# Optimization experiments

Hardware: AMD Instinct MI355X
Metric: run time of the kernel (lower is better)

## Reference

```python
import jax, jax.numpy as jnp
import numpy as np

N_NODES = 50000
N_EDGES = 800000
D_IN = 64
D_HID = 256
BN_EPS = 1e-5


def setup_inputs() -> dict:
    key = jax.random.key(0)
    ks = jax.random.split(key, 8)
    s = 1.0 / np.sqrt(D_IN)
    sg = 1.0 / np.sqrt(D_HID)
    return {
        "xs": jax.random.normal(ks[0], (N_NODES, D_IN), jnp.float32),
        "edge_index": jax.random.randint(ks[1], (2, N_EDGES), 0, N_NODES, jnp.int64),
        "W_gcn": jax.random.normal(ks[2], (D_IN, D_HID), jnp.float32) * s,
        "b_gcn": jnp.zeros((D_HID,), jnp.float32),
        "W_lin": jax.random.normal(ks[3], (D_IN, D_HID), jnp.float32) * s,
        "b_lin": jnp.zeros((D_HID,), jnp.float32),
        "W_gate": jax.random.normal(ks[4], (D_HID, D_HID), jnp.float32) * sg,
        "b_gate": jnp.zeros((D_HID,), jnp.float32),
        "bn_gamma": jnp.ones((D_HID,), jnp.float32),
        "bn_beta": jnp.zeros((D_HID,), jnp.float32),
    }


def reference(xs, edge_index, W_gcn, b_gcn, W_lin, b_lin, W_gate, b_gate, bn_gamma, bn_beta):
    N = xs.shape[0]
    # --- GCNConv: add self loops, symmetric normalization D^-1/2 (A+I) D^-1/2 ---
    loops = jnp.arange(N, dtype=edge_index.dtype)
    src = jnp.concatenate([edge_index[0], loops])  # message sources
    dst = jnp.concatenate([edge_index[1], loops])  # aggregation targets
    deg = jax.ops.segment_sum(jnp.ones(src.shape, jnp.float32), dst, num_segments=N)
    dinv = jax.lax.rsqrt(jnp.maximum(deg, 1.0))  # deg >= 1 due to self loops
    norm = dinv[src] * dinv[dst]                 # [E+N]
    h = xs @ W_gcn                               # [N, D_HID]
    z = jax.ops.segment_sum(h[src] * norm[:, None], dst, num_segments=N) + b_gcn
    z = jnp.tanh(z)
    # --- gating + linear residual ---
    g = jax.nn.sigmoid(z @ W_gate + b_gate)
    xl = xs @ W_lin + b_lin
    out = jax.nn.relu((1.0 - g) * xl + g * z)
    # --- BatchNorm over nodes (training-mode batch statistics) ---
    mu = out.mean(axis=0)
    var = out.var(axis=0)
    out = (out - mu) * jax.lax.rsqrt(var + BN_EPS) * bn_gamma + bn_beta
    # dropout is identity in eval mode
    return out
```

## Files before the change

kernel.cpp:

```cpp
#include <hip/hip_runtime.h>
#include <math.h>

#define NN 50000
#define NE 800000
#define D_IN 64
#define D_HID 256
#define BN_EPS 1e-5f
#define ZSTR 264
#define SB 128
#define BCAP 64

typedef __attribute__((ext_vector_type(8))) short short8;
typedef __attribute__((ext_vector_type(4))) float f32x4;

static __device__ __forceinline__ unsigned short f2bf(float f) {
    unsigned int u = __builtin_bit_cast(unsigned int, f);
    u += 0x7FFFu + ((u >> 16) & 1u);
    return (unsigned short)(u >> 16);
}
static __device__ __forceinline__ float bf2f(unsigned short s) {
    unsigned int u = ((unsigned int)s) << 16;
    return __builtin_bit_cast(float, u);
}
static __device__ __forceinline__ float fast_sigmoid(float x) {
    return __builtin_amdgcn_rcpf(1.0f + __expf(-x));
}
static __device__ __forceinline__ float fast_tanh(float x) {
    return 1.0f - 2.0f * __builtin_amdgcn_rcpf(__expf(2.0f * x) + 1.0f);
}

static __device__ __forceinline__ long a_addr(int i, int k) {
    return ((long)((i >> 4) * 2 + (k >> 5)) << 9) + ((((k >> 3) & 3) * 16 + (i & 15)) << 3) + (k & 7);
}

__global__ __launch_bounds__(256) void k_pre(const float* __restrict__ W_gcn,
                      const float* __restrict__ W_lin, const float* __restrict__ W_gate,
                      unsigned short* __restrict__ Wp_gcn, unsigned short* __restrict__ Wp_lin,
                      unsigned short* __restrict__ Wp_gate,
                      const int* __restrict__ eidx, int* __restrict__ cnt,
                      unsigned short* __restrict__ csr, int E) {
    int idx = blockIdx.x * blockDim.x + threadIdx.x;
    if (idx < 98304) {
        const float* W;
        unsigned short* Wp;
        int KC, o;
        if (idx < 16384)      { W = W_gcn;  Wp = Wp_gcn;  KC = 2; o = idx; }
        else if (idx < 32768) { W = W_lin;  Wp = Wp_lin;  KC = 2; o = idx - 16384; }
        else                  { W = W_gate; Wp = Wp_gate; KC = 8; o = idx - 32768; }
        int j = o & 7;
        int lane = (o >> 3) & 63;
        int rest = o >> 9;
        int kc = rest % KC;
        int ct = rest / KC;
        int col = ct * 16 + (lane & 15);
        int k = kc * 32 + (lane >> 4) * 8 + j;
        Wp[o] = f2bf(W[k * D_HID + col]);
    }
    if (idx * 4 < E) {
        int4 s = *(const int4*)(eidx + idx * 4);
        int4 d = *(const int4*)(eidx + E + idx * 4);
        int r0 = atomicAdd(&cnt[d.x], 1);
        int r1 = atomicAdd(&cnt[d.y], 1);
        int r2 = atomicAdd(&cnt[d.z], 1);
        int r3 = atomicAdd(&cnt[d.w], 1);
        if (r0 < BCAP) csr[d.x * BCAP + r0] = (unsigned short)s.x;
        if (r1 < BCAP) csr[d.y * BCAP + r1] = (unsigned short)s.y;
        if (r2 < BCAP) csr[d.z * BCAP + r2] = (unsigned short)s.z;
        if (r3 < BCAP) csr[d.w * BCAP + r3] = (unsigned short)s.w;
    }
}

__global__ __launch_bounds__(256) void k_prep(const float* __restrict__ xs,
                           const int* __restrict__ cnt,
                           float* __restrict__ dinv, unsigned short* __restrict__ xscaled,
                           unsigned short* __restrict__ xs_p, int n) {
    int idx = blockIdx.x * blockDim.x + threadIdx.x;
    if (idx >= n * 8) {
        if (idx < n * 8 + 8) {
            short8 zv = (short8){0, 0, 0, 0, 0, 0, 0, 0};
            *(short8*)(xscaled + (long)n * D_IN + (idx - n * 8) * 8) = zv;
        }
        return;
    }
    int i = idx >> 3;
    int sub = idx & 7;
    float dv = rsqrtf(1.0f + (float)cnt[i]);
    if (sub == 0) dinv[i] = dv;
    const float* p = xs + (long)i * D_IN + sub * 8;
    float4 f0 = *(const float4*)p;
    float4 f1 = *(const float4*)(p + 4);
    float vals[8] = {f0.x, f0.y, f0.z, f0.w, f1.x, f1.y, f1.z, f1.w};
    short8 xsc, xsb;
#pragma unroll
    for (int j = 0; j < 8; j++) {
        xsc[j] = (short)f2bf(vals[j] * dv);
        xsb[j] = (short)f2bf(vals[j]);
    }
    *(short8*)(xscaled + (long)i * D_IN + sub * 8) = xsc;
    *(short8*)(xs_p + a_addr(i, sub * 8)) = xsb;
}

__global__ __launch_bounds__(256) void k_gather(const unsigned short* __restrict__ csr,
                                                const int* __restrict__ cnt,
                                                const unsigned short* __restrict__ xscaled,
                                                const float* __restrict__ dinv,
                                                unsigned short* __restrict__ agg_p, int n) {
    int wv = threadIdx.x >> 6;
    int lane = threadIdx.x & 63;
    int sub = lane & 7;
    int grp = lane >> 3;
    int i = blockIdx.x * 4 + wv;
    if (i >= n) return;
    int c = cnt[i];
    c = c < BCAP ? c : BCAP;
    float acc[8];
#pragma unroll
    for (int j = 0; j < 8; j++) acc[j] = 0.f;
    {
        int m = c;
        int idxv = (lane < m) ? (int)csr[i * BCAP + lane] : 0;
        int tmax = (m + 7) >> 3;
        for (int t = 0; t < tmax; t++) {
            int e = t * 8 + grp;
            int rowv = __shfl(idxv, e);
            int row = (e < m) ? rowv : n;
            short8 v = *(const short8*)(xscaled + (long)row * D_IN + sub * 8);
#pragma unroll
            for (int j = 0; j < 8; j++) acc[j] += bf2f((unsigned short)v[j]);
        }
    }
#pragma unroll
    for (int d = 8; d <= 32; d <<= 1)
#pragma unroll
        for (int j = 0; j < 8; j++) acc[j] += __shfl_xor(acc[j], d);
    if (grp == 0) {
        float dv = dinv[i];
        short8 sv = *(const short8*)(xscaled + (long)i * D_IN + sub * 8);
        short8 o;
#pragma unroll
        for (int j = 0; j < 8; j++)
            o[j] = (short)f2bf((acc[j] + bf2f((unsigned short)sv[j])) * dv);
        *(short8*)(agg_p + a_addr(i, sub * 8)) = o;
    }
}

__global__ __launch_bounds__(256, 4) void k_fused(const unsigned short* __restrict__ agg_p,
                        const unsigned short* __restrict__ xs_p,
                        const unsigned short* __restrict__ Wp_gcn,
                        const unsigned short* __restrict__ Wp_lin,
                        const unsigned short* __restrict__ Wp_gate,
                        const float* __restrict__ b_gcn,
                        const float* __restrict__ bg,
                        const float* __restrict__ bl,
                        unsigned short* __restrict__ out_pre,
                        int n) {
    __shared__ unsigned short z_lds[32 * ZSTR];

    int tid = threadIdx.x;
    int wv = tid >> 6;
    int lane = tid & 63;
    int l15 = lane & 15;
    int quad = lane >> 4;
    int rt0 = blockIdx.x * 2;

    short8 aggf[2][2], xsf[2][2];
#pragma unroll
    for (int r = 0; r < 2; r++)
#pragma unroll
        for (int kc = 0; kc < 2; kc++) {
            aggf[r][kc] = *(const short8*)(agg_p + ((long)((rt0 + r) * 2 + kc) << 9) + lane * 8);
            xsf[r][kc]  = *(const short8*)(xs_p  + ((long)((rt0 + r) * 2 + kc) << 9) + lane * 8);
        }

    {
        short8 wg[2][4];
#pragma unroll
        for (int kc = 0; kc < 2; kc++)
#pragma unroll
            for (int tn = 0; tn < 4; tn++)
                wg[kc][tn] = *(const short8*)(Wp_gcn + ((long)((wv * 4 + tn) * 2 + kc) << 9) + lane * 8);
        float bias[4];
#pragma unroll
        for (int tn = 0; tn < 4; tn++) bias[tn] = b_gcn[wv * 64 + tn * 16 + l15];
#pragma unroll
        for (int r = 0; r < 2; r++) {
            f32x4 accz[4];
#pragma unroll
            for (int c = 0; c < 4; c++) accz[c] = (f32x4){0.f, 0.f, 0.f, 0.f};
#pragma unroll
            for (int kc = 0; kc < 2; kc++)
#pragma unroll
                for (int tn = 0; tn < 4; tn++)
                    accz[tn] = __builtin_amdgcn_mfma_f32_16x16x32_bf16(aggf[r][kc], wg[kc][tn], accz[tn], 0, 0, 0);
#pragma unroll
            for (int tn = 0; tn < 4; tn++) {
                int col = wv * 64 + tn * 16 + l15;
#pragma unroll
                for (int r2 = 0; r2 < 4; r2++)
                    z_lds[(r * 16 + quad * 4 + r2) * ZSTR + col] = f2bf(fast_tanh(accz[tn][r2] + bias[tn]));
            }
        }
    }
    __syncthreads();

    uint2 o_pk[2][4];
    float bgc[4], blc[4];
#pragma unroll
    for (int tn = 0; tn < 4; tn++) {
        int col = wv * 64 + tn * 16 + l15;
        bgc[tn] = bg[col];
        blc[tn] = bl[col];
    }
#pragma unroll
    for (int tnp = 0; tnp < 2; tnp++) {
        f32x4 accl[2][2];
#pragma unroll
        for (int r = 0; r < 2; r++)
#pragma unroll
            for (int h = 0; h < 2; h++) accl[r][h] = (f32x4){0.f, 0.f, 0.f, 0.f};
#pragma unroll
        for (int kc = 0; kc < 2; kc++) {
            short8 wl0 = *(const short8*)(Wp_lin + ((long)((wv * 4 + tnp * 2 + 0) * 2 + kc) << 9) + lane * 8);
            short8 wl1 = *(const short8*)(Wp_lin + ((long)((wv * 4 + tnp * 2 + 1) * 2 + kc) << 9) + lane * 8);
#pragma unroll
            for (int r = 0; r < 2; r++) {
                accl[r][0] = __builtin_amdgcn_mfma_f32_16x16x32_bf16(xsf[r][kc], wl0, accl[r][0], 0, 0, 0);
                accl[r][1] = __builtin_amdgcn_mfma_f32_16x16x32_bf16(xsf[r][kc], wl1, accl[r][1], 0, 0, 0);
            }
        }
        f32x4 acc1[2][2];
#pragma unroll
        for (int r = 0; r < 2; r++)
#pragma unroll
            for (int h = 0; h < 2; h++) acc1[r][h] = (f32x4){0.f, 0.f, 0.f, 0.f};
#pragma unroll
        for (int kc = 0; kc < 8; kc++) {
            short8 w0 = *(const short8*)(Wp_gate + ((long)((wv * 4 + tnp * 2 + 0) * 8 + kc) << 9) + lane * 8);
            short8 w1 = *(const short8*)(Wp_gate + ((long)((wv * 4 + tnp * 2 + 1) * 8 + kc) << 9) + lane * 8);
#pragma unroll
            for (int r = 0; r < 2; r++) {
                short8 af = *(const short8*)(&z_lds[(r * 16 + l15) * ZSTR + kc * 32 + quad * 8]);
                acc1[r][0] = __builtin_amdgcn_mfma_f32_16x16x32_bf16(af, w0, acc1[r][0], 0, 0, 0);
                acc1[r][1] = __builtin_amdgcn_mfma_f32_16x16x32_bf16(af, w1, acc1[r][1], 0, 0, 0);
            }
        }
#pragma unroll
        for (int h = 0; h < 2; h++) {
            int tn = tnp * 2 + h;
            int col = wv * 64 + tn * 16 + l15;
#pragma unroll
            for (int r = 0; r < 2; r++) {
                unsigned short op4[4];
#pragma unroll
                for (int r2 = 0; r2 < 4; r2++) {
                    int rl = r * 16 + quad * 4 + r2;
                    float g = fast_sigmoid(acc1[r][h][r2] + bgc[tn]);
                    float zv = bf2f(z_lds[rl * ZSTR + col]);
                    float xv = accl[r][h][r2] + blc[tn];
                    float o = fmaxf((1.f - g) * xv + g * zv, 0.f);
                    op4[r2] = f2bf(o);
                }
                o_pk[r][tn].x = (unsigned int)op4[0] | ((unsigned int)op4[1] << 16);
                o_pk[r][tn].y = (unsigned int)op4[2] | ((unsigned int)op4[3] << 16);
            }
        }
    }
    __syncthreads();

#pragma unroll
    for (int r = 0; r < 2; r++)
#pragma unroll
        for (int tn = 0; tn < 4; tn++) {
            int col = wv * 64 + tn * 16 + l15;
            int rl = r * 16 + quad * 4;
            z_lds[(rl + 0) * ZSTR + col] = (unsigned short)(o_pk[r][tn].x & 0xFFFF);
            z_lds[(rl + 1) * ZSTR + col] = (unsigned short)(o_pk[r][tn].x >> 16);
            z_lds[(rl + 2) * ZSTR + col] = (unsigned short)(o_pk[r][tn].y & 0xFFFF);
            z_lds[(rl + 3) * ZSTR + col] = (unsigned short)(o_pk[r][tn].y >> 16);
        }
    __syncthreads();

#pragma unroll
    for (int it = 0; it < 4; it++) {
        int g = it * 2048 + tid * 8;
        int row = g >> 8;
        int col = g & 255;
        short8 v = *(const short8*)(&z_lds[row * ZSTR + col]);
        *(short8*)(out_pre + (long)(blockIdx.x * 32 + row) * D_HID + col) = v;
    }
    (void)n;
}

__global__ __launch_bounds__(256) void k_stats(const unsigned short* __restrict__ op,
                        float* __restrict__ colsum, float* __restrict__ colsumsq, int n) {
    __shared__ float reds[4][32][8];
    __shared__ float redq[4][32][8];
    int tid = threadIdx.x;
    int wv = tid >> 6;
    int lane = tid & 63;
    int cg = tid & 31;
    int rb = tid >> 5;
    float ls[8], lq[8];
#pragma unroll
    for (int j = 0; j < 8; j++) { ls[j] = 0.f; lq[j] = 0.f; }
    for (int row = blockIdx.x * 8 + rb; row < n; row += SB * 8) {
        short8 v = *(const short8*)(op + (long)row * D_HID + cg * 8);
#pragma unroll
        for (int j = 0; j < 8; j++) {
            float f = bf2f((unsigned short)v[j]);
            ls[j] += f;
            lq[j] += f * f;
        }
    }
#pragma unroll
    for (int j = 0; j < 8; j++) {
        ls[j] += __shfl_xor(ls[j], 32);
        lq[j] += __shfl_xor(lq[j], 32);
    }
    if (lane < 32) {
#pragma unroll
        for (int j = 0; j < 8; j++) {
            reds[wv][cg][j] = ls[j];
            redq[wv][cg][j] = lq[j];
        }
    }
    __syncthreads();
    if (wv == 0 && lane < 32) {
#pragma unroll
        for (int j = 0; j < 8; j++) {
            float s = reds[0][cg][j] + reds[1][cg][j] + reds[2][cg][j] + reds[3][cg][j];
            float q = redq[0][cg][j] + redq[1][cg][j] + redq[2][cg][j] + redq[3][cg][j];
            atomicAdd(&colsum[cg * 8 + j], s);
            atomicAdd(&colsumsq[cg * 8 + j], q);
        }
    }
}

__global__ __launch_bounds__(256) void k_bn_apply(const unsigned short* __restrict__ op,
                           float* __restrict__ out,
                           const float* __restrict__ colsum, const float* __restrict__ colsumsq,
                           const float* __restrict__ gamma, const float* __restrict__ beta,
                           int n, int total8) {
    int i8 = blockIdx.x * blockDim.x + threadIdx.x;
    if (i8 >= total8) return;
    long idx = (long)i8 * 8;
    short8 p = *(const short8*)(op + idx);
    int c = (int)(idx & (D_HID - 1));
    float inv_n = 1.0f / (float)n;
    float vo[8];
#pragma unroll
    for (int j = 0; j < 8; j++) {
        float mu = colsum[c + j] * inv_n;
        float var = colsumsq[c + j] * inv_n - mu * mu;
        float sc = gamma[c + j] * rsqrtf(var + BN_EPS);
        vo[j] = bf2f((unsigned short)p[j]) * sc + (beta[c + j] - mu * sc);
    }
    float4 v0 = {vo[0], vo[1], vo[2], vo[3]};
    float4 v1 = {vo[4], vo[5], vo[6], vo[7]};
    *(float4*)(out + idx) = v0;
    *(float4*)(out + idx + 4) = v1;
}

extern "C" void kernel_launch(void* const* d_in, const int* in_sizes, int n_in,
                              void* d_out, int out_size, void* d_ws, size_t ws_size,
                              hipStream_t stream) {
    const float* xs     = (const float*)d_in[0];
    const int*   eidx   = (const int*)d_in[1];
    const float* W_gcn  = (const float*)d_in[2];
    const float* b_gcn  = (const float*)d_in[3];
    const float* W_lin  = (const float*)d_in[4];
    const float* b_lin  = (const float*)d_in[5];
    const float* W_gate = (const float*)d_in[6];
    const float* b_gate = (const float*)d_in[7];
    const float* gamma  = (const float*)d_in[8];
    const float* beta   = (const float*)d_in[9];
    float* out = (float*)d_out;

    const int n = in_sizes[0] / D_IN;
    const int E = in_sizes[1] / 2;
    const int npad = (n + 63) & ~63;

    char* ws = (char*)d_ws;
    size_t off = 0;
    auto alloc = [&](size_t bytes) {
        char* p = ws + off;
        off += (bytes + 511) & ~(size_t)511;
        return p;
    };
    size_t zero_begin = off;
    int*            cnt      = (int*)alloc((size_t)n * 4);
    float*          colsum   = (float*)alloc(D_HID * 4);
    float*          colsumsq = (float*)alloc(D_HID * 4);
    size_t zero_end = off;
    unsigned short* csr      = (unsigned short*)alloc((size_t)n * BCAP * 2);
    float*          dinv     = (float*)alloc((size_t)n * 4);
    unsigned short* xscaled  = (unsigned short*)alloc((size_t)(n + 1) * D_IN * 2);
    unsigned short* xs_p     = (unsigned short*)alloc((size_t)npad * D_IN * 2);
    unsigned short* agg_p    = (unsigned short*)alloc((size_t)npad * D_IN * 2);
    unsigned short* out_pre  = (unsigned short*)alloc((size_t)npad * D_HID * 2);
    unsigned short* Wp_gcn   = (unsigned short*)alloc((size_t)D_IN * D_HID * 2);
    unsigned short* Wp_lin   = (unsigned short*)alloc((size_t)D_IN * D_HID * 2);
    unsigned short* Wp_gate  = (unsigned short*)alloc((size_t)D_HID * D_HID * 2);
    (void)ws_size;

    const int B = 256;

    hipMemsetAsync(ws + zero_begin, 0, zero_end - zero_begin, stream);
    k_pre<<<(E / 4 + B - 1) / B, B, 0, stream>>>(W_gcn, W_lin, W_gate, Wp_gcn, Wp_lin, Wp_gate,
                                                 eidx, cnt, csr, E);
    k_prep<<<(n * 8 + 8 + B - 1) / B, B, 0, stream>>>(xs, cnt, dinv, xscaled, xs_p, n);
    k_gather<<<(n + 3) / 4, B, 0, stream>>>(csr, cnt, xscaled, dinv, agg_p, n);
    k_fused<<<npad / 32, B, 0, stream>>>(agg_p, xs_p, Wp_gcn, Wp_lin, Wp_gate,
                                         b_gcn, b_gate, b_lin, out_pre, n);
    k_stats<<<SB, B, 0, stream>>>(out_pre, colsum, colsumsq, n);
    {
        int total8 = n * D_HID / 8;
        k_bn_apply<<<(total8 + B - 1) / B, B, 0, stream>>>(out_pre, out, colsum, colsumsq,
                                                           gamma, beta, n, total8);
    }
}
```

Baseline: 240.7 us.

## Build CSR via two-pass binning by destination block instead of global atomics

Replaces the per-edge global atomicAdd CSR construction with a two-stage scheme. First, edges are binned by destination>>8 using shared-memory counters and one global atomic per bin per block. Then a new kernel assembles each bin's CSR slice in LDS and writes it out with coalesced stores. This targets scattered global atomics and random 2-byte writes, at the cost of an extra launch, an intermediate binbuf, and a fixed bin capacity that could drop edges on skewed inputs.

```diff
diff --git a/kernel.cpp b/kernel.cpp
--- a/kernel.cpp
+++ b/kernel.cpp
@@ -9,6 +9,7 @@
 #define ZSTR 264
 #define SB 128
 #define BCAP 64
+#define BINCAP 8192
 
 typedef __attribute__((ext_vector_type(8))) short short8;
 typedef __attribute__((ext_vector_type(4))) float f32x4;
@@ -37,8 +38,8 @@
                       const float* __restrict__ W_lin, const float* __restrict__ W_gate,
                       unsigned short* __restrict__ Wp_gcn, unsigned short* __restrict__ Wp_lin,
                       unsigned short* __restrict__ Wp_gate,
-                      const int* __restrict__ eidx, int* __restrict__ cnt,
-                      unsigned short* __restrict__ csr, int E) {
+                      const int* __restrict__ eidx, int* __restrict__ bincur,
+                      unsigned int* __restrict__ binbuf, int E) {
     int idx = blockIdx.x * blockDim.x + threadIdx.x;
     if (idx < 98304) {
         const float* W;
@@ -56,17 +57,79 @@
         int k = kc * 32 + (lane >> 4) * 8 + j;
         Wp[o] = f2bf(W[k * D_HID + col]);
     }
-    if (idx * 4 < E) {
-        int4 s = *(const int4*)(eidx + idx * 4);
-        int4 d = *(const int4*)(eidx + E + idx * 4);
-        int r0 = atomicAdd(&cnt[d.x], 1);
-        int r1 = atomicAdd(&cnt[d.y], 1);
-        int r2 = atomicAdd(&cnt[d.z], 1);
-        int r3 = atomicAdd(&cnt[d.w], 1);
-        if (r0 < BCAP) csr[d.x * BCAP + r0] = (unsigned short)s.x;
-        if (r1 < BCAP) csr[d.y * BCAP + r1] = (unsigned short)s.y;
-        if (r2 < BCAP) csr[d.z * BCAP + r2] = (unsigned short)s.z;
-        if (r3 < BCAP) csr[d.w * BCAP + r3] = (unsigned short)s.w;
+
+    int b = blockIdx.x;
+    int t = threadIdx.x;
+    int nbb = (E + 4095) >> 12;
+    if (b < nbb) {
+        __shared__ int bcnt[256];
+        __shared__ int gbase[256];
+        bcnt[t] = 0;
+        __syncthreads();
+        unsigned int pair[4][4];
+        int bin[4][4], lr[4][4];
+        bool val[4];
+#pragma unroll
+        for (int c = 0; c < 4; c++) {
+            int e0 = b * 4096 + c * 1024 + t * 4;
+            val[c] = e0 < E;
+            if (val[c]) {
+                int4 s = *(const int4*)(eidx + e0);
+                int4 d = *(const int4*)(eidx + E + e0);
+                int ss[4] = {s.x, s.y, s.z, s.w};
+                int dd[4] = {d.x, d.y, d.z, d.w};
+#pragma unroll
+                for (int j = 0; j < 4; j++) {
+                    int bi = dd[j] >> 8;
+                    bin[c][j] = bi;
+                    pair[c][j] = ((unsigned int)(dd[j] & 255) << 16) | (unsigned int)ss[j];
+                    lr[c][j] = atomicAdd(&bcnt[bi], 1);
+                }
+            }
+        }
+        __syncthreads();
+        if (bcnt[t] > 0) gbase[t] = atomicAdd(&bincur[t], bcnt[t]);
+        __syncthreads();
+#pragma unroll
+        for (int c = 0; c < 4; c++)
+            if (val[c]) {
+#pragma unroll
+                for (int j = 0; j < 4; j++) {
+                    int slot = gbase[bin[c][j]] + lr[c][j];
+                    if (slot < BINCAP)
+                        binbuf[((long)bin[c][j] << 13) + slot] = pair[c][j];
+                }
+            }
+    }
+}
+
+__global__ __launch_bounds__(256) void k_binfill(const unsigned int* __restrict__ binbuf,
+                      const int* __restrict__ bincur,
+                      unsigned short* __restrict__ csr, int* __restrict__ cnt, int n) {
+    __shared__ unsigned short buck[256 * BCAP];
+    __shared__ int lcnt[256];
+    int b = blockIdx.x;
+    int t = threadIdx.x;
+    lcnt[t] = 0;
+    __syncthreads();
+    int tot = bincur[b];
+    tot = tot < BINCAP ? tot : BINCAP;
+    for (int i = t; i < tot; i += 256) {
+        unsigned int p = binbuf[((long)b << 13) + i];
+        int dl = p >> 16;
+        int src = p & 0xFFFF;
+        int r = atomicAdd(&lcnt[dl], 1);
+        if (r < BCAP) buck[dl * BCAP + r] = (unsigned short)src;
+    }
+    __syncthreads();
+    int node0 = b << 8;
+    if (node0 + t < n) cnt[node0 + t] = lcnt[t];
+#pragma unroll
+    for (int v = 0; v < 8; v++) {
+        int e = (v * 256 + t) * 8;
+        int node = e >> 6;
+        if (node0 + node < n)
+            *(short8*)(csr + ((long)(node0 + node) << 6) + (e & 63)) = *(const short8*)(&buck[e]);
     }
 }
 
@@ -379,6 +442,7 @@
     const int n = in_sizes[0] / D_IN;
     const int E = in_sizes[1] / 2;
     const int npad = (n + 63) & ~63;
+    const int nbins = (n + 255) >> 8;
 
     char* ws = (char*)d_ws;
     size_t off = 0;
@@ -388,10 +452,12 @@
         return p;
     };
     size_t zero_begin = off;
-    int*            cnt      = (int*)alloc((size_t)n * 4);
+    int*            bincur   = (int*)alloc(256 * 4);
     float*          colsum   = (float*)alloc(D_HID * 4);
     float*          colsumsq = (float*)alloc(D_HID * 4);
     size_t zero_end = off;
+    int*            cnt      = (int*)alloc((size_t)n * 4);
+    unsigned int*   binbuf   = (unsigned int*)alloc((size_t)nbins * BINCAP * 4);
     unsigned short* csr      = (unsigned short*)alloc((size_t)n * BCAP * 2);
     float*          dinv     = (float*)alloc((size_t)n * 4);
     unsigned short* xscaled  = (unsigned short*)alloc((size_t)(n + 1) * D_IN * 2);
@@ -406,8 +472,9 @@
     const int B = 256;
 
     hipMemsetAsync(ws + zero_begin, 0, zero_end - zero_begin, stream);
-    k_pre<<<(E / 4 + B - 1) / B, B, 0, stream>>>(W_gcn, W_lin, W_gate, Wp_gcn, Wp_lin, Wp_gate,
-                                                 eidx, cnt, csr, E);
+    k_pre<<<384, B, 0, stream>>>(W_gcn, W_lin, W_gate, Wp_gcn, Wp_lin, Wp_gate,
+                                 eidx, bincur, binbuf, E);
+    k_binfill<<<nbins, B, 0, stream>>>(binbuf, bincur, csr, cnt, n);
     k_prep<<<(n * 8 + 8 + B - 1) / B, B, 0, stream>>>(xs, cnt, dinv, xscaled, xs_p, n);
     k_gather<<<(n + 3) / 4, B, 0, stream>>>(csr, cnt, xscaled, dinv, agg_p, n);
     k_fused<<<npad / 32, B, 0, stream>>>(agg_p, xs_p, Wp_gcn, Wp_lin, Wp_gate,
```

Result: faster. 214.5 us (-10.9%).
